# Performance work log

Hardware: AMD Instinct MI355X
Metric: run time of the kernel (lower is better)

Reference implementation:

```python
import jax, jax.numpy as jnp
import numpy as np

N_COLS = 107
CAT_SLICES = [(1, 10), (10, 26), (27, 34), (34, 49), (49, 55), (55, 60), (60, 62), (65, 107)]
MSE_COLS = [0, 26, 62, 63, 64]
BATCH = 524288


def setup_inputs() -> dict:
    key = jax.random.key(0)
    k_dec, k_cont, k_cat = jax.random.split(key, 3)
    data_decoded = jax.random.normal(k_dec, (BATCH, N_COLS), dtype=jnp.float32)
    # Build data_true: continuous cols random, categorical slices exactly one-hot.
    data_true = jax.random.uniform(k_cont, (BATCH, N_COLS), dtype=jnp.float32)
    rows = jnp.arange(BATCH)
    for i, (s, e) in enumerate(CAT_SLICES):
        kk = jax.random.fold_in(k_cat, i)
        labels = jax.random.randint(kk, (BATCH,), 0, e - s)
        data_true = data_true.at[:, s:e].set(0.0)
        data_true = data_true.at[rows, s + labels].set(1.0)
    return {"data_decoded": data_decoded, "data_true": data_true, "batch_size": BATCH}


def _ce(logits, onehot_true):
    # torch nonzero()[:,1] on an exact one-hot slice == argmax
    labels = jnp.argmax(onehot_true, axis=1)
    logp = jax.nn.log_softmax(logits, axis=1)
    return -jnp.mean(jnp.take_along_axis(logp, labels[:, None], axis=1))


def _mse(a, b):
    d = a - b
    return jnp.mean(d * d)


def reference(data_decoded, data_true, batch_size):
    mse_loss = jnp.float32(0.0)
    for c in MSE_COLS:
        mse_loss = mse_loss + _mse(data_decoded[:, c], data_true[:, c])
    ce_loss = jnp.float32(0.0)
    for s, e in CAT_SLICES:
        ce_loss = ce_loss + _ce(data_decoded[:, s:e], data_true[:, s:e])
    multi_loss = mse_loss + ce_loss
    return multi_loss, mse_loss, ce_loss
```

## Files before the change

### kernel.cpp

```cpp
#include <hip/hip_runtime.h>

#define NCOLS 107

template<int S, int E>
__device__ __forceinline__ float slice_ce(const float* __restrict__ dr,
                                          const float* __restrict__ tr) {
    constexpr int L = E - S;
    float v[L];
#pragma unroll
    for (int j = 0; j < L; ++j) v[j] = dr[S + j];
    float m = v[0];
#pragma unroll
    for (int j = 1; j < L; ++j) m = fmaxf(m, v[j]);
    float sum = 0.0f, dot = 0.0f;
#pragma unroll
    for (int j = 0; j < L; ++j) {
        sum += __expf(v[j] - m);
        dot = fmaf(v[j], tr[S + j], dot);
    }
    return m + __logf(sum) - dot;
}

__global__ __launch_bounds__(256) void multiloss_main(
        const float* __restrict__ dec, const float* __restrict__ tru,
        float* __restrict__ ws, int nrows) {
    int row = blockIdx.x * blockDim.x + threadIdx.x;
    float mse = 0.0f, ce = 0.0f;
    if (row < nrows) {
        const float* dr = dec + (size_t)row * NCOLS;
        const float* tr = tru + (size_t)row * NCOLS;
        float d;
        d = dr[0]  - tr[0];  mse = fmaf(d, d, mse);
        d = dr[26] - tr[26]; mse = fmaf(d, d, mse);
        d = dr[62] - tr[62]; mse = fmaf(d, d, mse);
        d = dr[63] - tr[63]; mse = fmaf(d, d, mse);
        d = dr[64] - tr[64]; mse = fmaf(d, d, mse);
        ce += slice_ce<1, 10>(dr, tr);
        ce += slice_ce<10, 26>(dr, tr);
        ce += slice_ce<27, 34>(dr, tr);
        ce += slice_ce<34, 49>(dr, tr);
        ce += slice_ce<49, 55>(dr, tr);
        ce += slice_ce<55, 60>(dr, tr);
        ce += slice_ce<60, 62>(dr, tr);
        ce += slice_ce<65, 107>(dr, tr);
    }
#pragma unroll
    for (int off = 32; off > 0; off >>= 1) {
        mse += __shfl_down(mse, off, 64);
        ce  += __shfl_down(ce,  off, 64);
    }
    __shared__ float smse[4], sce[4];
    int wid  = threadIdx.x >> 6;
    int lane = threadIdx.x & 63;
    if (lane == 0) { smse[wid] = mse; sce[wid] = ce; }
    __syncthreads();
    if (threadIdx.x == 0) {
        float bm = smse[0] + smse[1] + smse[2] + smse[3];
        float bc = sce[0]  + sce[1]  + sce[2]  + sce[3];
        atomicAdd(&ws[0], bm);
        atomicAdd(&ws[1], bc);
    }
}

__global__ void multiloss_fin(const float* __restrict__ ws,
                              float* __restrict__ out, float invN) {
    float mse = ws[0] * invN;
    float ce  = ws[1] * invN;
    out[0] = mse + ce;
    out[1] = mse;
    out[2] = ce;
}

extern "C" void kernel_launch(void* const* d_in, const int* in_sizes, int n_in,
                              void* d_out, int out_size, void* d_ws, size_t ws_size,
                              hipStream_t stream) {
    const float* dec = (const float*)d_in[0];
    const float* tru = (const float*)d_in[1];
    int nrows = in_sizes[0] / NCOLS;
    float* ws = (float*)d_ws;
    hipMemsetAsync(ws, 0, 2 * sizeof(float), stream);
    int blocks = (nrows + 255) / 256;
    multiloss_main<<<blocks, 256, 0, stream>>>(dec, tru, ws, nrows);
    multiloss_fin<<<1, 1, 0, stream>>>(ws, (float*)d_out, 1.0f / (float)nrows);
}
```

Before: 515.1 us.

## Stage row tiles in LDS with coalesced float4 loads and split slices across threads

```diff
diff --git a/kernel.cpp b/kernel.cpp
--- a/kernel.cpp
+++ b/kernel.cpp
@@ -1,10 +1,12 @@
 #include <hip/hip_runtime.h>
 
 #define NCOLS 107
+#define TROWS 64
+#define TELEMS (TROWS * NCOLS)
+#define TVEC  (TELEMS / 4)
 
 template<int S, int E>
-__device__ __forceinline__ float slice_ce(const float* __restrict__ dr,
-                                          const float* __restrict__ tr) {
+__device__ __forceinline__ float slice_ce_lds(const float* dr, const float* tr) {
     constexpr int L = E - S;
     float v[L];
 #pragma unroll
@@ -21,29 +23,64 @@
     return m + __logf(sum) - dot;
 }
 
-__global__ __launch_bounds__(256) void multiloss_main(
+__global__ __launch_bounds__(256, 2) void multiloss_main(
         const float* __restrict__ dec, const float* __restrict__ tru,
-        float* __restrict__ ws, int nrows) {
-    int row = blockIdx.x * blockDim.x + threadIdx.x;
+        float2* __restrict__ ws, int nrows) {
+    __shared__ float4 sdec4[TVEC];
+    __shared__ float4 stru4[TVEC];
+    const float* sdec = (const float*)sdec4;
+    const float* stru = (const float*)stru4;
+
+    int tile0 = blockIdx.x * TROWS;
+    int rows_here = nrows - tile0;
+    if (rows_here > TROWS) rows_here = TROWS;
+    size_t base = (size_t)tile0 * NCOLS;
+
+    if (rows_here == TROWS) {
+        const float4* gd = (const float4*)(dec + base);
+        const float4* gt = (const float4*)(tru + base);
+        for (int i = threadIdx.x; i < TVEC; i += 256) {
+            sdec4[i] = gd[i];
+            stru4[i] = gt[i];
+        }
+    } else {
+        int n = rows_here * NCOLS;
+        float* sd = (float*)sdec4;
+        float* st = (float*)stru4;
+        for (int i = threadIdx.x; i < n; i += 256) {
+            sd[i] = dec[base + i];
+            st[i] = tru[base + i];
+        }
+    }
+    __syncthreads();
+
+    int row  = threadIdx.x >> 2;
+    int part = threadIdx.x & 3;
     float mse = 0.0f, ce = 0.0f;
-    if (row < nrows) {
-        const float* dr = dec + (size_t)row * NCOLS;
-        const float* tr = tru + (size_t)row * NCOLS;
-        float d;
-        d = dr[0]  - tr[0];  mse = fmaf(d, d, mse);
-        d = dr[26] - tr[26]; mse = fmaf(d, d, mse);
-        d = dr[62] - tr[62]; mse = fmaf(d, d, mse);
-        d = dr[63] - tr[63]; mse = fmaf(d, d, mse);
-        d = dr[64] - tr[64]; mse = fmaf(d, d, mse);
-        ce += slice_ce<1, 10>(dr, tr);
-        ce += slice_ce<10, 26>(dr, tr);
-        ce += slice_ce<27, 34>(dr, tr);
-        ce += slice_ce<34, 49>(dr, tr);
-        ce += slice_ce<49, 55>(dr, tr);
-        ce += slice_ce<55, 60>(dr, tr);
-        ce += slice_ce<60, 62>(dr, tr);
-        ce += slice_ce<65, 107>(dr, tr);
+    if (row < rows_here) {
+        const float* dr = sdec + row * NCOLS;
+        const float* tr = stru + row * NCOLS;
+        if (part == 0) {
+            ce += slice_ce_lds<65, 107>(dr, tr);
+        } else if (part == 1) {
+            ce += slice_ce_lds<10, 26>(dr, tr);
+            ce += slice_ce_lds<34, 49>(dr, tr);
+        } else if (part == 2) {
+            ce += slice_ce_lds<1, 10>(dr, tr);
+            ce += slice_ce_lds<27, 34>(dr, tr);
+            ce += slice_ce_lds<49, 55>(dr, tr);
+        } else {
+            ce += slice_ce_lds<55, 60>(dr, tr);
+            ce += slice_ce_lds<60, 62>(dr, tr);
+            float d;
+            d = dr[0]  - tr[0];  mse = fmaf(d, d, mse);
+            d = dr[26] - tr[26]; mse = fmaf(d, d, mse);
+            d = dr[62] - tr[62]; mse = fmaf(d, d, mse);
+            d = dr[63] - tr[63]; mse = fmaf(d, d, mse);
+            d = dr[64] - tr[64]; mse = fmaf(d, d, mse);
+        }
     }
+
 #pragma unroll
     for (int off = 32; off > 0; off >>= 1) {
         mse += __shfl_down(mse, off, 64);
@@ -57,18 +94,35 @@
     if (threadIdx.x == 0) {
         float bm = smse[0] + smse[1] + smse[2] + smse[3];
         float bc = sce[0]  + sce[1]  + sce[2]  + sce[3];
-        atomicAdd(&ws[0], bm);
-        atomicAdd(&ws[1], bc);
+        ws[blockIdx.x] = make_float2(bm, bc);
     }
 }
 
-__global__ void multiloss_fin(const float* __restrict__ ws,
-                              float* __restrict__ out, float invN) {
-    float mse = ws[0] * invN;
-    float ce  = ws[1] * invN;
-    out[0] = mse + ce;
-    out[1] = mse;
-    out[2] = ce;
+__global__ __launch_bounds__(256) void multiloss_fin(
+        const float2* __restrict__ ws, float* __restrict__ out,
+        int nblocks, float invN) {
+    float m = 0.0f, c = 0.0f;
+    for (int i = threadIdx.x; i < nblocks; i += 256) {
+        float2 v = ws[i];
+        m += v.x; c += v.y;
+    }
+#pragma unroll
+    for (int off = 32; off > 0; off >>= 1) {
+        m += __shfl_down(m, off, 64);
+        c += __shfl_down(c, off, 64);
+    }
+    __shared__ float sm[4], sc[4];
+    int wid  = threadIdx.x >> 6;
+    int lane = threadIdx.x & 63;
+    if (lane == 0) { sm[wid] = m; sc[wid] = c; }
+    __syncthreads();
+    if (threadIdx.x == 0) {
+        float mse = (sm[0] + sm[1] + sm[2] + sm[3]) * invN;
+        float ce  = (sc[0] + sc[1] + sc[2] + sc[3]) * invN;
+        out[0] = mse + ce;
+        out[1] = mse;
+        out[2] = ce;
+    }
 }
 
 extern "C" void kernel_launch(void* const* d_in, const int* in_sizes, int n_in,
@@ -77,9 +131,9 @@
     const float* dec = (const float*)d_in[0];
     const float* tru = (const float*)d_in[1];
     int nrows = in_sizes[0] / NCOLS;
-    float* ws = (float*)d_ws;
-    hipMemsetAsync(ws, 0, 2 * sizeof(float), stream);
-    int blocks = (nrows + 255) / 256;
-    multiloss_main<<<blocks, 256, 0, stream>>>(dec, tru, ws, nrows);
-    multiloss_fin<<<1, 1, 0, stream>>>(ws, (float*)d_out, 1.0f / (float)nrows);
+    int nblocks = (nrows + TROWS - 1) / TROWS;
+    float2* ws = (float2*)d_ws;
+    multiloss_main<<<nblocks, 256, 0, stream>>>(dec, tru, ws, nrows);
+    multiloss_fin<<<1, 256, 0, stream>>>(ws, (float*)d_out, nblocks,
+                                         1.0f / (float)nrows);
 }
```

Result: faster. 460.2 us (-10.7%).

## Vectorize row loads with streaming softmax and grid-stride partial-sum reduction

Applied to the files above, without the earlier changes.

```diff
diff --git a/kernel.cpp b/kernel.cpp
--- a/kernel.cpp
+++ b/kernel.cpp
@@ -1,74 +1,120 @@
 #include <hip/hip_runtime.h>
+#include <float.h>
 
 #define NCOLS 107
+#define THREADS 256
+#define BLOCKS 2048
 
-template<int S, int E>
-__device__ __forceinline__ float slice_ce(const float* __restrict__ dr,
-                                          const float* __restrict__ tr) {
-    constexpr int L = E - S;
-    float v[L];
-#pragma unroll
-    for (int j = 0; j < L; ++j) v[j] = dr[S + j];
-    float m = v[0];
-#pragma unroll
-    for (int j = 1; j < L; ++j) m = fmaxf(m, v[j]);
-    float sum = 0.0f, dot = 0.0f;
-#pragma unroll
-    for (int j = 0; j < L; ++j) {
-        sum += __expf(v[j] - m);
-        dot = fmaf(v[j], tr[S + j], dot);
-    }
-    return m + __logf(sum) - dot;
+typedef float f4 __attribute__((ext_vector_type(4)));
+
+__device__ __forceinline__ int col_class(int c) {
+    if (c == 0 || c == 26 || (c >= 62 && c <= 64)) return -1;
+    if (c < 10) return 0;
+    if (c < 26) return 1;
+    if (c < 34) return 2;
+    if (c < 49) return 3;
+    if (c < 55) return 4;
+    if (c < 60) return 5;
+    if (c < 62) return 6;
+    return 7;
 }
 
-__global__ __launch_bounds__(256) void multiloss_main(
+struct RowState {
+    float m[8], s[8], mse, dot;
+};
+
+__device__ __forceinline__ void proc(int c, float d, float t, RowState& st) {
+    int k = col_class(c);
+    if (k < 0) {
+        float df = d - t;
+        st.mse = fmaf(df, df, st.mse);
+    } else {
+        st.dot = fmaf(d, t, st.dot);
+        float mn = fmaxf(st.m[k], d);
+        st.s[k] = fmaf(st.s[k], __expf(st.m[k] - mn), __expf(d - mn));
+        st.m[k] = mn;
+    }
+}
+
+__device__ __forceinline__ f4 ld4(const float* p) {
+    f4 v;
+    __builtin_memcpy(&v, p, 16);
+    return v;
+}
+
+__global__ __launch_bounds__(THREADS) void multiloss_main(
         const float* __restrict__ dec, const float* __restrict__ tru,
-        float* __restrict__ ws, int nrows) {
-    int row = blockIdx.x * blockDim.x + threadIdx.x;
-    float mse = 0.0f, ce = 0.0f;
-    if (row < nrows) {
+        float2* __restrict__ ws, int nrows) {
+    int tid    = blockIdx.x * THREADS + threadIdx.x;
+    int stride = gridDim.x * THREADS;
+
+    float mse = 0.0f, dot = 0.0f, lsesum = 0.0f;
+
+    for (int row = tid; row < nrows; row += stride) {
         const float* dr = dec + (size_t)row * NCOLS;
         const float* tr = tru + (size_t)row * NCOLS;
-        float d;
-        d = dr[0]  - tr[0];  mse = fmaf(d, d, mse);
-        d = dr[26] - tr[26]; mse = fmaf(d, d, mse);
-        d = dr[62] - tr[62]; mse = fmaf(d, d, mse);
-        d = dr[63] - tr[63]; mse = fmaf(d, d, mse);
-        d = dr[64] - tr[64]; mse = fmaf(d, d, mse);
-        ce += slice_ce<1, 10>(dr, tr);
-        ce += slice_ce<10, 26>(dr, tr);
-        ce += slice_ce<27, 34>(dr, tr);
-        ce += slice_ce<34, 49>(dr, tr);
-        ce += slice_ce<49, 55>(dr, tr);
-        ce += slice_ce<55, 60>(dr, tr);
-        ce += slice_ce<60, 62>(dr, tr);
-        ce += slice_ce<65, 107>(dr, tr);
+        RowState st;
+#pragma unroll
+        for (int k = 0; k < 8; ++k) { st.m[k] = -FLT_MAX; st.s[k] = 0.0f; }
+        st.mse = 0.0f; st.dot = 0.0f;
+
+#pragma unroll
+        for (int g = 0; g < 26; ++g) {
+            f4 dv = ld4(dr + 4 * g);
+            f4 tv = ld4(tr + 4 * g);
+            proc(4 * g + 0, dv.x, tv.x, st);
+            proc(4 * g + 1, dv.y, tv.y, st);
+            proc(4 * g + 2, dv.z, tv.z, st);
+            proc(4 * g + 3, dv.w, tv.w, st);
+        }
+        {
+            f4 dv = ld4(dr + 103);
+            f4 tv = ld4(tr + 103);
+            proc(104, dv.y, tv.y, st);
+            proc(105, dv.z, tv.z, st);
+            proc(106, dv.w, tv.w, st);
+        }
+#pragma unroll
+        for (int k = 0; k < 8; ++k) lsesum += st.m[k] + __logf(st.s[k]);
+        mse += st.mse;
+        dot += st.dot;
     }
+
+    float ce = lsesum - dot;
 #pragma unroll
     for (int off = 32; off > 0; off >>= 1) {
         mse += __shfl_down(mse, off, 64);
         ce  += __shfl_down(ce,  off, 64);
     }
-    __shared__ float smse[4], sce[4];
+    if ((threadIdx.x & 63) == 0)
+        ws[tid >> 6] = make_float2(mse, ce);
+}
+
+__global__ __launch_bounds__(256) void multiloss_fin(
+        const float2* __restrict__ ws, float* __restrict__ out,
+        int nslots, float invN) {
+    float m = 0.0f, c = 0.0f;
+    for (int i = threadIdx.x; i < nslots; i += 256) {
+        float2 v = ws[i];
+        m += v.x; c += v.y;
+    }
+#pragma unroll
+    for (int off = 32; off > 0; off >>= 1) {
+        m += __shfl_down(m, off, 64);
+        c += __shfl_down(c, off, 64);
+    }
+    __shared__ float sm[4], sc[4];
     int wid  = threadIdx.x >> 6;
     int lane = threadIdx.x & 63;
-    if (lane == 0) { smse[wid] = mse; sce[wid] = ce; }
+    if (lane == 0) { sm[wid] = m; sc[wid] = c; }
     __syncthreads();
     if (threadIdx.x == 0) {
-        float bm = smse[0] + smse[1] + smse[2] + smse[3];
-        float bc = sce[0]  + sce[1]  + sce[2]  + sce[3];
-        atomicAdd(&ws[0], bm);
-        atomicAdd(&ws[1], bc);
+        float mse = (sm[0] + sm[1] + sm[2] + sm[3]) * invN;
+        float ce  = (sc[0] + sc[1] + sc[2] + sc[3]) * invN;
+        out[0] = mse + ce;
+        out[1] = mse;
+        out[2] = ce;
     }
-}
-
-__global__ void multiloss_fin(const float* __restrict__ ws,
-                              float* __restrict__ out, float invN) {
-    float mse = ws[0] * invN;
-    float ce  = ws[1] * invN;
-    out[0] = mse + ce;
-    out[1] = mse;
-    out[2] = ce;
 }
 
 extern "C" void kernel_launch(void* const* d_in, const int* in_sizes, int n_in,
@@ -76,10 +122,10 @@
                               hipStream_t stream) {
     const float* dec = (const float*)d_in[0];
     const float* tru = (const float*)d_in[1];
-    int nrows = in_sizes[0] / NCOLS;
-    float* ws = (float*)d_ws;
-    hipMemsetAsync(ws, 0, 2 * sizeof(float), stream);
-    int blocks = (nrows + 255) / 256;
-    multiloss_main<<<blocks, 256, 0, stream>>>(dec, tru, ws, nrows);
-    multiloss_fin<<<1, 1, 0, stream>>>(ws, (float*)d_out, 1.0f / (float)nrows);
+    int nrows  = in_sizes[0] / NCOLS;
+    int nslots = BLOCKS * THREADS / 64;
+    float2* ws = (float2*)d_ws;
+    multiloss_main<<<BLOCKS, THREADS, 0, stream>>>(dec, tru, ws, nrows);
+    multiloss_fin<<<1, 256, 0, stream>>>(ws, (float*)d_out, nslots,
+                                         1.0f / (float)nrows);
 }
```

Measured after the change: 503.7 us. 1.02x faster.
